# Kernel optimization log

Measured on AMD Instinct MI355X. Metric: run time of the kernel, lower is better.

## Reference

```python
import jax, jax.numpy as jnp
import numpy as np

BN_EPS = 1e-5


def _bn_relu(h, gamma, beta):
    # BatchNorm1d in training mode: normalize over (batch, length) per channel
    mean = h.mean(axis=(0, 2), keepdims=True)
    var = h.var(axis=(0, 2), keepdims=True)
    h = (h - mean) * jax.lax.rsqrt(var + BN_EPS)
    h = h * gamma[None, :, None] + beta[None, :, None]
    return jax.nn.relu(h)


def _gather(ldesc, idx):
    # ldesc: [B, D, N], idx: [B, M] -> [B, D, M]
    B, D, N = ldesc.shape
    M = idx.shape[1]
    return jnp.take_along_axis(ldesc, jnp.broadcast_to(idx[:, None, :], (B, D, M)), axis=2)


def _scatter_mean(src, idx, N):
    # per-batch scatter-mean: src [B, D, M], idx [B, M] -> [B, D, N]
    def one(s, i):
        D = s.shape[0]
        sums = jnp.zeros((D, N), s.dtype).at[:, i].add(s)
        cnts = jnp.zeros((N,), s.dtype).at[i].add(1.0)
        return sums / jnp.maximum(cnts, 1.0)[None, :]
    return jax.vmap(one)(src, idx)


def _endpoint_update(ldesc, line_enc, idx, W1, b1, g1, bt1, W2, b2):
    B, D, _ = ldesc.shape
    ld = _gather(ldesc, idx)                                   # [B, D, 2L]
    # flip endpoint pairs: neighbor endpoint of each endpoint
    neigh = ld.reshape(B, D, -1, 2)[..., ::-1].reshape(B, D, -1)
    msg = jnp.concatenate([ld, neigh, line_enc], axis=1)       # [B, 3D, 2L]
    h = jnp.einsum('oc,bcm->bom', W1, msg) + b1[None, :, None]  # Conv1d k=1
    h = _bn_relu(h, g1, bt1)
    out = jnp.einsum('oc,bcm->bom', W2, h) + b2[None, :, None]
    return out                                                  # [B, D, 2L]


def setup_inputs() -> dict:
    key = jax.random.key(0)
    ks = jax.random.split(key, 12)
    B, D, N, M = 8, 256, 8192, 8192
    inp = {
        'ldesc0': jax.random.normal(ks[0], (B, D, N), jnp.float32),
        'ldesc1': jax.random.normal(ks[1], (B, D, N), jnp.float32),
        'line_enc0': jax.random.normal(ks[2], (B, D, M), jnp.float32),
        'line_enc1': jax.random.normal(ks[3], (B, D, M), jnp.float32),
        'lines_junc_idx0': jax.random.randint(ks[4], (B, M), 0, N),
        'lines_junc_idx1': jax.random.randint(ks[5], (B, M), 0, N),
        'W1': jax.random.normal(ks[6], (2 * D, 3 * D), jnp.float32) * (1.0 / np.sqrt(3 * D)),
        'b1': jnp.zeros((2 * D,), jnp.float32),
        'g1': jnp.ones((2 * D,), jnp.float32),
        'bt1': jnp.zeros((2 * D,), jnp.float32),
        'W2': jax.random.normal(ks[7], (D, 2 * D), jnp.float32) * (1.0 / np.sqrt(2 * D)),
        'b2': jnp.zeros((D,), jnp.float32),
    }
    return inp


def reference(ldesc0, ldesc1, line_enc0, line_enc1, lines_junc_idx0, lines_junc_idx1,
              W1, b1, g1, bt1, W2, b2):
    N = ldesc0.shape[2]
    up0 = _endpoint_update(ldesc0, line_enc0, lines_junc_idx0, W1, b1, g1, bt1, W2, b2)
    up1 = _endpoint_update(ldesc1, line_enc1, lines_junc_idx1, W1, b1, g1, bt1, W2, b2)
    out0 = ldesc0 + _scatter_mean(up0, lines_junc_idx0, N)
    out1 = ldesc1 + _scatter_mean(up1, lines_junc_idx1, N)
    return (out0, out1)
```

## Files before the change

### kernel.cpp

```cpp
#include <hip/hip_runtime.h>
#include <hip/hip_bf16.h>

#define B_  8
#define D_  256
#define N_  8192
#define M_  8192
#define O1_ 512
#define K1_ 768
#define K2_ 512

typedef unsigned short u16;
typedef __attribute__((ext_vector_type(8))) short bf8;
typedef __attribute__((ext_vector_type(4))) float f4;

static __device__ __forceinline__ float bf2f(u16 u) {
    unsigned v = ((unsigned)u) << 16;
    return __uint_as_float(v);
}
static __device__ __forceinline__ u16 f2bf(float f) {
    __hip_bfloat16 h = __float2bfloat16(f);
    return *reinterpret_cast<u16*>(&h);
}
static __device__ __forceinline__ void gl_lds16(const u16* g, u16* l) {
    __builtin_amdgcn_global_load_lds((const __attribute__((address_space(1))) void*)g,
                                     (__attribute__((address_space(3))) void*)l, 16, 0, 0);
}
static __device__ __forceinline__ int swz64(int r) {
    return (((r >> 1) & 1) << 4) | (((r >> 2) & 1) << 5);
}

__global__ __launch_bounds__(256) void k_transpose_bf16(const float* __restrict__ src,
                                                        u16* __restrict__ dst, int R, int C) {
    __shared__ float t[32][33];
    const int b  = blockIdx.z;
    const int c0 = blockIdx.x * 32, r0 = blockIdx.y * 32;
    const int tx = threadIdx.x, ty = threadIdx.y;
    const float* s = src + (size_t)b * R * C;
    u16* d = dst + (size_t)b * C * R;
#pragma unroll
    for (int i = 0; i < 4; ++i) {
        int r = r0 + ty + i * 8;
        t[ty + i * 8][tx] = s[(size_t)r * C + (c0 + tx)];
    }
    __syncthreads();
#pragma unroll
    for (int i = 0; i < 4; ++i) {
        int c = c0 + ty + i * 8;
        d[(size_t)c * R + (r0 + tx)] = f2bf(t[tx][ty + i * 8]);
    }
}

__global__ __launch_bounds__(256) void k_convert_w(const float* __restrict__ W1, const float* __restrict__ W2,
                                                   u16* __restrict__ W1b, u16* __restrict__ W2b) {
    int i = blockIdx.x * 256 + threadIdx.x;
    const int n1 = O1_ * K1_;
    const int n2 = D_ * K2_;
    if (i < n1) W1b[i] = f2bf(W1[i]);
    int j = i - n1;
    if (j >= 0 && j < n2) W2b[j] = f2bf(W2[j]);
}

#define NT1 12
__global__ __launch_bounds__(512, 2) void k_gemm1(const u16* __restrict__ W1b,
                                                  const u16* __restrict__ Tld,
                                                  const u16* __restrict__ Tle,
                                                  const int* __restrict__ idx,
                                                  u16* __restrict__ hbuf) {
    __shared__ u16 LA[2][2][256][32];
    __shared__ u16 LB[2][2][256][32];
    const int b  = blockIdx.z;
    const int o0 = blockIdx.y * 256;
    const int m0 = blockIdx.x * 256;
    const int tid = threadIdx.x;
    const int w = tid >> 6, l = tid & 63;
    const int wr = w >> 2;
    const int wc = w & 3;

    const int srow   = tid >> 2;
    const int schunk = (tid & 3) * 16;

    int na[2], nb[2], mm[2];
    const u16* aS[2];
    int bcolu[2];
#pragma unroll
    for (int j = 0; j < 2; ++j) {
        int r = j * 128 + srow;
        int m = m0 + r;
        mm[j] = m;
        na[j] = idx[b * M_ + m];
        nb[j] = idx[b * M_ + (m ^ 1)];
        int swu = (schunk ^ swz64(r)) >> 1;
        aS[j]   = W1b + (size_t)(o0 + r) * K1_ + swu;
        bcolu[j] = swu;
    }

    int aOff[8], bOff[4];
#pragma unroll
    for (int i = 0; i < 8; ++i) {
        int r = wr * 128 + i * 16 + (l & 15);
        aOff[i] = r * 32 + ((((l >> 4) * 16) ^ swz64(r)) >> 1);
    }
#pragma unroll
    for (int j = 0; j < 4; ++j) {
        int r = wc * 64 + j * 16 + (l & 15);
        bOff[j] = r * 32 + ((((l >> 4) * 16) ^ swz64(r)) >> 1);
    }

#define STAGE_A1(kt, ks, buf)                                                        \
    {                                                                                \
        _Pragma("unroll")                                                            \
        for (int j = 0; j < 2; ++j)                                                  \
            gl_lds16(aS[j] + (kt) * 64 + (ks) * 32, &LA[buf][ks][j * 128][0] + tid * 8); \
    }
#define STAGE_B1(kt, ks, buf)                                                        \
    {                                                                                \
        const int seg = (kt) >> 2;                                                   \
        const int cb  = ((kt) & 3) * 64 + (ks) * 32;                                 \
        _Pragma("unroll")                                                            \
        for (int j = 0; j < 2; ++j) {                                                \
            const u16* s;                                                            \
            if (seg == 0)      s = Tld + (size_t)(b * N_ + na[j]) * D_ + cb + bcolu[j]; \
            else if (seg == 1) s = Tld + (size_t)(b * N_ + nb[j]) * D_ + cb + bcolu[j]; \
            else               s = Tle + (size_t)(b * M_ + mm[j]) * D_ + cb + bcolu[j]; \
            gl_lds16(s, &LB[buf][ks][j * 128][0] + tid * 8);                         \
        }                                                                            \
    }

    f4 acc[8][4];
#pragma unroll
    for (int i = 0; i < 8; ++i)
#pragma unroll
        for (int j = 0; j < 4; ++j) acc[i][j] = {0.f, 0.f, 0.f, 0.f};

    STAGE_A1(0, 0, 0); STAGE_B1(0, 0, 0);
    STAGE_A1(0, 1, 0); STAGE_B1(0, 1, 0);
    STAGE_A1(1, 0, 1); STAGE_B1(1, 0, 1);
    asm volatile("s_waitcnt vmcnt(8)" ::: "memory");
    __builtin_amdgcn_s_barrier();
    __builtin_amdgcn_sched_barrier(0);

    for (int t = 0; t < NT1; ++t) {
        const int bufp = t & 1, nbuf = bufp ^ 1;
        const u16* baseA0 = &LA[bufp][0][0][0];
        const u16* baseA1 = &LA[bufp][1][0][0];
        const u16* baseB0 = &LB[bufp][0][0][0];
        const u16* baseB1 = &LB[bufp][1][0][0];
        bf8 aF[4], bF[4];

#pragma unroll
        for (int j = 0; j < 4; ++j) bF[j] = *reinterpret_cast<const bf8*>(baseB0 + bOff[j]);
#pragma unroll
        for (int ii = 0; ii < 4; ++ii) aF[ii] = *reinterpret_cast<const bf8*>(baseA0 + aOff[ii]);
        if (t + 1 < NT1) STAGE_A1(t + 1, 1, nbuf);
        __builtin_amdgcn_s_barrier();
        asm volatile("s_waitcnt lgkmcnt(0)" ::: "memory");
        __builtin_amdgcn_sched_barrier(0);
        __builtin_amdgcn_s_setprio(1);
#pragma unroll
        for (int ii = 0; ii < 4; ++ii)
#pragma unroll
            for (int j = 0; j < 4; ++j)
                acc[ii][j] = __builtin_amdgcn_mfma_f32_16x16x32_bf16(aF[ii], bF[j], acc[ii][j], 0, 0, 0);
        __builtin_amdgcn_s_setprio(0);
        __builtin_amdgcn_s_barrier();
        __builtin_amdgcn_sched_barrier(0);

#pragma unroll
        for (int ii = 0; ii < 4; ++ii) aF[ii] = *reinterpret_cast<const bf8*>(baseA0 + aOff[4 + ii]);
        if (t + 1 < NT1) STAGE_B1(t + 1, 1, nbuf);
        __builtin_amdgcn_s_barrier();
        asm volatile("s_waitcnt lgkmcnt(0)" ::: "memory");
        __builtin_amdgcn_sched_barrier(0);
        __builtin_amdgcn_s_setprio(1);
#pragma unroll
        for (int ii = 0; ii < 4; ++ii)
#pragma unroll
            for (int j = 0; j < 4; ++j)
                acc[4 + ii][j] = __builtin_amdgcn_mfma_f32_16x16x32_bf16(aF[ii], bF[j], acc[4 + ii][j], 0, 0, 0);
        __builtin_amdgcn_s_setprio(0);
        if (t < NT1 - 2) asm volatile("s_waitcnt vmcnt(8)" ::: "memory");
        else             asm volatile("s_waitcnt vmcnt(0)" ::: "memory");
        __builtin_amdgcn_s_barrier();
        __builtin_amdgcn_sched_barrier(0);

#pragma unroll
        for (int j = 0; j < 4; ++j) bF[j] = *reinterpret_cast<const bf8*>(baseB1 + bOff[j]);
#pragma unroll
        for (int ii = 0; ii < 4; ++ii) aF[ii] = *reinterpret_cast<const bf8*>(baseA1 + aOff[ii]);
        if (t + 2 < NT1) STAGE_A1(t + 2, 0, bufp);
        __builtin_amdgcn_s_barrier();
        asm volatile("s_waitcnt lgkmcnt(0)" ::: "memory");
        __builtin_amdgcn_sched_barrier(0);
        __builtin_amdgcn_s_setprio(1);
#pragma unroll
        for (int ii = 0; ii < 4; ++ii)
#pragma unroll
            for (int j = 0; j < 4; ++j)
                acc[ii][j] = __builtin_amdgcn_mfma_f32_16x16x32_bf16(aF[ii], bF[j], acc[ii][j], 0, 0, 0);
        __builtin_amdgcn_s_setprio(0);
        __builtin_amdgcn_s_barrier();
        __builtin_amdgcn_sched_barrier(0);

#pragma unroll
        for (int ii = 0; ii < 4; ++ii) aF[ii] = *reinterpret_cast<const bf8*>(baseA1 + aOff[4 + ii]);
        if (t + 2 < NT1) STAGE_B1(t + 2, 0, bufp);
        __builtin_amdgcn_s_barrier();
        asm volatile("s_waitcnt lgkmcnt(0)" ::: "memory");
        __builtin_amdgcn_sched_barrier(0);
        __builtin_amdgcn_s_setprio(1);
#pragma unroll
        for (int ii = 0; ii < 4; ++ii)
#pragma unroll
            for (int j = 0; j < 4; ++j)
                acc[4 + ii][j] = __builtin_amdgcn_mfma_f32_16x16x32_bf16(aF[ii], bF[j], acc[4 + ii][j], 0, 0, 0);
        __builtin_amdgcn_s_setprio(0);
        if (t < NT1 - 2) asm volatile("s_waitcnt vmcnt(8)" ::: "memory");
        else             asm volatile("s_waitcnt vmcnt(0)" ::: "memory");
        __builtin_amdgcn_s_barrier();
        __builtin_amdgcn_sched_barrier(0);
    }
#undef STAGE_A1
#undef STAGE_B1

#pragma unroll
    for (int j = 0; j < 4; ++j) {
        int m = m0 + wc * 64 + j * 16 + (l & 15);
        size_t rowbase = (size_t)(b * M_ + m) * O1_;
#pragma unroll
        for (int i = 0; i < 8; ++i) {
            int orow = o0 + wr * 128 + i * 16 + (l >> 4) * 4;
            ushort4 pk;
            pk.x = f2bf(acc[i][j].x);
            pk.y = f2bf(acc[i][j].y);
            pk.z = f2bf(acc[i][j].z);
            pk.w = f2bf(acc[i][j].w);
            *reinterpret_cast<ushort4*>(&hbuf[rowbase + orow]) = pk;
        }
    }
}

__global__ __launch_bounds__(256) void k_stats(const u16* __restrict__ hbuf, float* __restrict__ stats) {
    const int t = threadIdx.x;
    const size_t row0 = (size_t)blockIdx.x * 256;
    float s0 = 0.f, q0 = 0.f, s1 = 0.f, q1 = 0.f;
    for (int r = 0; r < 256; ++r) {
        const u16* p = hbuf + (row0 + r) * O1_;
        float v0 = bf2f(p[t]);
        float v1 = bf2f(p[t + 256]);
        s0 += v0; q0 += v0 * v0;
        s1 += v1; q1 += v1 * v1;
    }
    atomicAdd(&stats[t], s0);
    atomicAdd(&stats[O1_ + t], q0);
    atomicAdd(&stats[t + 256], s1);
    atomicAdd(&stats[O1_ + t + 256], q1);
}

__global__ void k_finalize_ac(const float* __restrict__ stats, const float* __restrict__ g1,
                              const float* __restrict__ bt1, float* __restrict__ ac) {
    int o = blockIdx.x * 256 + threadIdx.x;
    if (o >= O1_) return;
    const float inv = 1.0f / ((float)B_ * (float)M_);
    float mean = stats[o] * inv;
    float var  = stats[O1_ + o] * inv - mean * mean;
    var = fmaxf(var, 0.0f);
    float a = g1[o] * rsqrtf(var + 1e-5f);
    ac[o] = a;
    ac[O1_ + o] = bt1[o] - mean * a;
}

__global__ void k_count_int(const int* __restrict__ idx, int* __restrict__ cnt) {
    int i = blockIdx.x * 256 + threadIdx.x;
    if (i < B_ * M_) atomicAdd(&cnt[(i >> 13) * N_ + idx[i]], 1);
}

__global__ __launch_bounds__(1024) void k_scan(const int* __restrict__ cnt, int* __restrict__ offs,
                                               int* __restrict__ fill) {
    __shared__ int wsum[1024];
    const int b = blockIdx.x;
    const int t = threadIdx.x;
    const int base = b * N_;
    int v[8]; int s = 0;
#pragma unroll
    for (int k = 0; k < 8; ++k) { v[k] = cnt[base + t * 8 + k]; s += v[k]; }
    wsum[t] = s;
    __syncthreads();
    for (int off = 1; off < 1024; off <<= 1) {
        int add = (t >= off) ? wsum[t - off] : 0;
        __syncthreads();
        wsum[t] += add;
        __syncthreads();
    }
    int run = (t > 0) ? wsum[t - 1] : 0;
#pragma unroll
    for (int k = 0; k < 8; ++k) {
        offs[base + t * 8 + k] = run;
        fill[base + t * 8 + k] = run;
        run += v[k];
    }
}

__global__ void k_fill(const int* __restrict__ idx, int* __restrict__ fill, int* __restrict__ mlist) {
    int i = blockIdx.x * 256 + threadIdx.x;
    if (i < B_ * M_) {
        int b = i >> 13, m = i & (M_ - 1);
        int pos = atomicAdd(&fill[b * N_ + idx[i]], 1);
        mlist[(size_t)b * M_ + pos] = m;
    }
}

__global__ __launch_bounds__(256) void k_gemm2(const u16* __restrict__ W2b,
                                               const u16* __restrict__ hbuf,
                                               const float* __restrict__ ac,
                                               const float* __restrict__ b2,
                                               u16* __restrict__ up) {
    __shared__ u16 At[128 * 32];
    __shared__ u16 Bt[128 * 32];
    __shared__ float acs[1024];
    const int b  = blockIdx.z;
    const int d0 = blockIdx.y * 128;
    const int m0 = blockIdx.x * 128;
    const int tid = threadIdx.x;
    const int w = tid >> 6, l = tid & 63;
    const int lr = l >> 2, lc = (l & 3) * 8;

    acs[tid]       = ac[tid];
    acs[tid + 256] = ac[tid + 256];
    acs[tid + 512] = ac[tid + 512];
    acs[tid + 768] = ac[tid + 768];

    const u16* pA[2]; const u16* pB[2];
#pragma unroll
    for (int t = 0; t < 2; ++t) {
        int row = t * 64 + w * 16 + lr;
        pA[t] = W2b + (size_t)(d0 + row) * K2_ + lc;
        int m  = m0 + row;
        pB[t] = hbuf + (size_t)(b * M_ + m) * O1_ + lc;
    }
    const int wr = w >> 1, wc = w & 1;
    f4 acc[4][4];
#pragma unroll
    for (int i = 0; i < 4; ++i)
#pragma unroll
        for (int j = 0; j < 4; ++j) acc[i][j] = {0.f, 0.f, 0.f, 0.f};

    const int aoff = (wr * 64 + (l & 15)) * 32 + (l >> 4) * 8;
    const int boff = (wc * 64 + (l & 15)) * 32 + (l >> 4) * 8;
    const int bdst = (w * 16 + lr) * 32 + lc;

    __syncthreads();

    for (int kk = 0; kk < 16; ++kk) {
        const int o = kk * 32 + lc;
        f4 A0 = *reinterpret_cast<const f4*>(&acs[o]);
        f4 A1 = *reinterpret_cast<const f4*>(&acs[o + 4]);
        f4 C0 = *reinterpret_cast<const f4*>(&acs[512 + o]);
        f4 C1 = *reinterpret_cast<const f4*>(&acs[512 + o + 4]);
#pragma unroll
        for (int t = 0; t < 2; ++t) {
            gl_lds16(pA[t] + kk * 32, At + (t * 64 + w * 16) * 32);
            const ushort4* ps = reinterpret_cast<const ushort4*>(pB[t] + kk * 32);
            ushort4 v0 = ps[0], v1 = ps[1];
            union { ushort4 u4[2]; bf8 v8; } pk;
            pk.u4[0].x = f2bf(fmaxf(bf2f(v0.x) * A0.x + C0.x, 0.0f));
            pk.u4[0].y = f2bf(fmaxf(bf2f(v0.y) * A0.y + C0.y, 0.0f));
            pk.u4[0].z = f2bf(fmaxf(bf2f(v0.z) * A0.z + C0.z, 0.0f));
            pk.u4[0].w = f2bf(fmaxf(bf2f(v0.w) * A0.w + C0.w, 0.0f));
            pk.u4[1].x = f2bf(fmaxf(bf2f(v1.x) * A1.x + C1.x, 0.0f));
            pk.u4[1].y = f2bf(fmaxf(bf2f(v1.y) * A1.y + C1.y, 0.0f));
            pk.u4[1].z = f2bf(fmaxf(bf2f(v1.z) * A1.z + C1.z, 0.0f));
            pk.u4[1].w = f2bf(fmaxf(bf2f(v1.w) * A1.w + C1.w, 0.0f));
            *reinterpret_cast<bf8*>(&Bt[t * 64 * 32 + bdst]) = pk.v8;
        }
        __syncthreads();
        bf8 aF[4], bF[4];
#pragma unroll
        for (int i = 0; i < 4; ++i) aF[i] = *reinterpret_cast<const bf8*>(&At[aoff + i * 16 * 32]);
#pragma unroll
        for (int j = 0; j < 4; ++j) bF[j] = *reinterpret_cast<const bf8*>(&Bt[boff + j * 16 * 32]);
#pragma unroll
        for (int i = 0; i < 4; ++i)
#pragma unroll
            for (int j = 0; j < 4; ++j)
                acc[i][j] = __builtin_amdgcn_mfma_f32_16x16x32_bf16(aF[i], bF[j], acc[i][j], 0, 0, 0);
        __syncthreads();
    }

#pragma unroll
    for (int j = 0; j < 4; ++j) {
        int m = m0 + wc * 64 + j * 16 + (l & 15);
        size_t rowbase = (size_t)(b * M_ + m) * D_;
#pragma unroll
        for (int i = 0; i < 4; ++i) {
            int d = d0 + wr * 64 + i * 16 + (l >> 4) * 4;
            ushort4 pk;
            pk.x = f2bf(acc[i][j].x + b2[d + 0]);
            pk.y = f2bf(acc[i][j].y + b2[d + 1]);
            pk.z = f2bf(acc[i][j].z + b2[d + 2]);
            pk.w = f2bf(acc[i][j].w + b2[d + 3]);
            *reinterpret_cast<ushort4*>(&up[rowbase + d]) = pk;
        }
    }
}

__global__ __launch_bounds__(256) void k_reduce_finalize(const float* __restrict__ ldesc,
                                                         const u16* __restrict__ up,
                                                         const int* __restrict__ cnt,
                                                         const int* __restrict__ offs,
                                                         const int* __restrict__ mlist,
                                                         float* __restrict__ out) {
    __shared__ float lds[32][257];
    const int b  = blockIdx.z;
    const int n0 = blockIdx.x * 32;
    const int tx = threadIdx.x, ty = threadIdx.y;
#pragma unroll
    for (int i = 0; i < 4; ++i) {
        int nl = ty + i * 8;
        int n  = n0 + nl;
        int c   = cnt[b * N_ + n];
        int off = offs[b * N_ + n];
        float inv = 1.0f / (float)max(c, 1);
        float acc[8] = {0.f, 0.f, 0.f, 0.f, 0.f, 0.f, 0.f, 0.f};
        for (int e = 0; e < c; ++e) {
            int m = mlist[(size_t)b * M_ + off + e];
            const ushort4* row = reinterpret_cast<const ushort4*>(up + (size_t)(b * M_ + m) * D_ + tx * 8);
            ushort4 aa = row[0], bb = row[1];
            acc[0] += bf2f(aa.x); acc[1] += bf2f(aa.y); acc[2] += bf2f(aa.z); acc[3] += bf2f(aa.w);
            acc[4] += bf2f(bb.x); acc[5] += bf2f(bb.y); acc[6] += bf2f(bb.z); acc[7] += bf2f(bb.w);
        }
#pragma unroll
        for (int k = 0; k < 8; ++k) lds[nl][tx * 8 + k] = acc[k] * inv;
    }
    __syncthreads();
#pragma unroll
    for (int i = 0; i < 32; ++i) {
        int d = ty + i * 8;
        size_t o2 = (size_t)(b * D_ + d) * N_ + n0 + tx;
        out[o2] = ldesc[o2] + lds[tx][d];
    }
}

__global__ void k_marker(float* out, float v) { out[0] = v; }

extern "C" void kernel_launch(void* const* d_in, const int* in_sizes, int n_in,
                              void* d_out, int out_size, void* d_ws, size_t ws_size,
                              hipStream_t stream) {
    const float* ldesc0 = (const float*)d_in[0];
    const float* ldesc1 = (const float*)d_in[1];
    const float* le0    = (const float*)d_in[2];
    const float* le1    = (const float*)d_in[3];
    const int*   idx0   = (const int*)d_in[4];
    const int*   idx1   = (const int*)d_in[5];
    const float* W1     = (const float*)d_in[6];
    const float* g1     = (const float*)d_in[8];
    const float* bt1    = (const float*)d_in[9];
    const float* W2     = (const float*)d_in[10];
    const float* b2     = (const float*)d_in[11];
    float* out = (float*)d_out;

    char* ws = (char*)d_ws;
    const size_t oTld   = 0;
    const size_t oTle   = 33554432;
    const size_t oH     = 67108864;
    const size_t oW1b   = 134217728;
    const size_t oW2b   = oW1b + 786432;
    const size_t oStats = oW2b + 262144;
    const size_t oAC    = oStats + 4096;
    const size_t NEED   = oAC + 4096;
    if (ws_size < NEED) {
        k_marker<<<1, 1, 0, stream>>>(out, 1000.0f + (float)(ws_size >> 20));
        return;
    }
    u16*   Tld   = (u16*)(ws + oTld);
    u16*   up    = (u16*)(ws + oTld);
    u16*   Tle   = (u16*)(ws + oTle);
    int*   cnt   = (int*)(ws + oTle);
    int*   offs  = (int*)(ws + oTle + 262144);
    int*   fill  = (int*)(ws + oTle + 524288);
    int*   mlist = (int*)(ws + oTle + 786432);
    u16*   hbuf  = (u16*)(ws + oH);
    u16*   W1b   = (u16*)(ws + oW1b);
    u16*   W2b   = (u16*)(ws + oW2b);
    float* stats = (float*)(ws + oStats);
    float* ac    = (float*)(ws + oAC);

    k_convert_w<<<2048, 256, 0, stream>>>(W1, W2, W1b, W2b);

    const dim3 tb(32, 8);
    for (int s = 0; s < 2; ++s) {
        const float* ld  = s ? ldesc1 : ldesc0;
        const float* le  = s ? le1 : le0;
        const int*   idx = s ? idx1 : idx0;
        float* outp = out + (size_t)s * B_ * D_ * N_;

        k_transpose_bf16<<<dim3(N_ / 32, D_ / 32, B_), tb, 0, stream>>>(ld, Tld, D_, N_);
        k_transpose_bf16<<<dim3(M_ / 32, D_ / 32, B_), tb, 0, stream>>>(le, Tle, D_, M_);
        k_gemm1<<<dim3(M_ / 256, O1_ / 256, B_), 512, 0, stream>>>(W1b, Tld, Tle, idx, hbuf);
        hipMemsetAsync(stats, 0, 4096, stream);
        k_stats<<<256, 256, 0, stream>>>(hbuf, stats);
        k_finalize_ac<<<2, 256, 0, stream>>>(stats, g1, bt1, ac);
        hipMemsetAsync(cnt, 0, (size_t)B_ * N_ * 4, stream);
        k_count_int<<<B_ * M_ / 256, 256, 0, stream>>>(idx, cnt);
        k_scan<<<B_, 1024, 0, stream>>>(cnt, offs, fill);
        k_fill<<<B_ * M_ / 256, 256, 0, stream>>>(idx, fill, mlist);
        k_gemm2<<<dim3(M_ / 128, D_ / 128, B_), 256, 0, stream>>>(W2b, hbuf, ac, b2, up);
        k_reduce_finalize<<<dim3(N_ / 32, 1, B_), tb, 0, stream>>>(ld, up, cnt, offs, mlist, outp);
    }
}
```

Measured before the change: 453.4 us.

## Batch both sides into single kernel launches with doubled workspace

Replaces the two-iteration per-side loop with single launches that cover both sides through an extra grid dimension. Each kernel now picks its side from blockIdx.z, and the workspace buffers are doubled to hold both sides. This cuts the launch count roughly in half and gives larger grids, so small kernels such as scan, stats and finalize fill the GPU better. The cost is twice the workspace memory and a larger working set per kernel, which can hurt cache reuse.

Result: faster. 412.9 us (-8.9%).

```diff
diff --git a/kernel.cpp b/kernel.cpp
--- a/kernel.cpp
+++ b/kernel.cpp
@@ -29,24 +29,28 @@
     return (((r >> 1) & 1) << 4) | (((r >> 2) & 1) << 5);
 }
 
-__global__ __launch_bounds__(256) void k_transpose_bf16(const float* __restrict__ src,
-                                                        u16* __restrict__ dst, int R, int C) {
+__global__ __launch_bounds__(256) void k_transpose_all(const float* __restrict__ s0, const float* __restrict__ s1,
+                                                       const float* __restrict__ s2, const float* __restrict__ s3,
+                                                       u16* __restrict__ dA, u16* __restrict__ dB) {
     __shared__ float t[32][33];
-    const int b  = blockIdx.z;
+    const int z = blockIdx.z;
+    const int sel = z >> 3, b = z & 7;
+    const float* src = (sel == 0) ? s0 : (sel == 1) ? s1 : (sel == 2) ? s2 : s3;
+    u16* dst = ((sel < 2) ? dA : dB) + (size_t)(sel & 1) * B_ * N_ * D_;
     const int c0 = blockIdx.x * 32, r0 = blockIdx.y * 32;
     const int tx = threadIdx.x, ty = threadIdx.y;
-    const float* s = src + (size_t)b * R * C;
-    u16* d = dst + (size_t)b * C * R;
+    const float* s = src + (size_t)b * D_ * N_;
+    u16* d = dst + (size_t)b * N_ * D_;
 #pragma unroll
     for (int i = 0; i < 4; ++i) {
         int r = r0 + ty + i * 8;
-        t[ty + i * 8][tx] = s[(size_t)r * C + (c0 + tx)];
+        t[ty + i * 8][tx] = s[(size_t)r * N_ + (c0 + tx)];
     }
     __syncthreads();
 #pragma unroll
     for (int i = 0; i < 4; ++i) {
         int c = c0 + ty + i * 8;
-        d[(size_t)c * R + (r0 + tx)] = f2bf(t[tx][ty + i * 8]);
+        d[(size_t)c * D_ + (r0 + tx)] = f2bf(t[tx][ty + i * 8]);
     }
 }
 
@@ -62,13 +66,19 @@
 
 #define NT1 12
 __global__ __launch_bounds__(512, 2) void k_gemm1(const u16* __restrict__ W1b,
-                                                  const u16* __restrict__ Tld,
-                                                  const u16* __restrict__ Tle,
-                                                  const int* __restrict__ idx,
-                                                  u16* __restrict__ hbuf) {
+                                                  const u16* __restrict__ Tld2,
+                                                  const u16* __restrict__ Tle2,
+                                                  const int* __restrict__ idx0,
+                                                  const int* __restrict__ idx1,
+                                                  u16* __restrict__ hbuf2) {
     __shared__ u16 LA[2][2][256][32];
     __shared__ u16 LB[2][2][256][32];
-    const int b  = blockIdx.z;
+    const int z  = blockIdx.z;
+    const int side = z >> 3, b = z & 7;
+    const u16* Tld = Tld2 + (size_t)side * B_ * N_ * D_;
+    const u16* Tle = Tle2 + (size_t)side * B_ * N_ * D_;
+    const int* idx = side ? idx1 : idx0;
+    u16* hbuf = hbuf2 + (size_t)side * B_ * M_ * O1_;
     const int o0 = blockIdx.y * 256;
     const int m0 = blockIdx.x * 256;
     const int tid = threadIdx.x;
@@ -239,50 +249,59 @@
     }
 }
 
-__global__ __launch_bounds__(256) void k_stats(const u16* __restrict__ hbuf, float* __restrict__ stats) {
+__global__ __launch_bounds__(256) void k_stats(const u16* __restrict__ hbuf2, float* __restrict__ stats) {
+    const int side = blockIdx.x >> 8;
+    const int blk  = blockIdx.x & 255;
+    const u16* hb = hbuf2 + (size_t)side * B_ * M_ * O1_;
+    float* st = stats + side * 1024;
     const int t = threadIdx.x;
-    const size_t row0 = (size_t)blockIdx.x * 256;
+    const size_t row0 = (size_t)blk * 256;
     float s0 = 0.f, q0 = 0.f, s1 = 0.f, q1 = 0.f;
     for (int r = 0; r < 256; ++r) {
-        const u16* p = hbuf + (row0 + r) * O1_;
+        const u16* p = hb + (row0 + r) * O1_;
         float v0 = bf2f(p[t]);
         float v1 = bf2f(p[t + 256]);
         s0 += v0; q0 += v0 * v0;
         s1 += v1; q1 += v1 * v1;
     }
-    atomicAdd(&stats[t], s0);
-    atomicAdd(&stats[O1_ + t], q0);
-    atomicAdd(&stats[t + 256], s1);
-    atomicAdd(&stats[O1_ + t + 256], q1);
+    atomicAdd(&st[t], s0);
+    atomicAdd(&st[O1_ + t], q0);
+    atomicAdd(&st[t + 256], s1);
+    atomicAdd(&st[O1_ + t + 256], q1);
 }
 
 __global__ void k_finalize_ac(const float* __restrict__ stats, const float* __restrict__ g1,
                               const float* __restrict__ bt1, float* __restrict__ ac) {
-    int o = blockIdx.x * 256 + threadIdx.x;
-    if (o >= O1_) return;
+    int i = blockIdx.x * 256 + threadIdx.x;
+    if (i >= 1024) return;
+    int side = i >> 9, o = i & 511;
+    const float* st = stats + side * 1024;
     const float inv = 1.0f / ((float)B_ * (float)M_);
-    float mean = stats[o] * inv;
-    float var  = stats[O1_ + o] * inv - mean * mean;
+    float mean = st[o] * inv;
+    float var  = st[O1_ + o] * inv - mean * mean;
     var = fmaxf(var, 0.0f);
     float a = g1[o] * rsqrtf(var + 1e-5f);
-    ac[o] = a;
-    ac[O1_ + o] = bt1[o] - mean * a;
-}
-
-__global__ void k_count_int(const int* __restrict__ idx, int* __restrict__ cnt) {
+    ac[side * 1024 + o] = a;
+    ac[side * 1024 + O1_ + o] = bt1[o] - mean * a;
+}
+
+__global__ void k_count_int(const int* __restrict__ idx0, const int* __restrict__ idx1, int* __restrict__ cnt2) {
     int i = blockIdx.x * 256 + threadIdx.x;
-    if (i < B_ * M_) atomicAdd(&cnt[(i >> 13) * N_ + idx[i]], 1);
-}
-
-__global__ __launch_bounds__(1024) void k_scan(const int* __restrict__ cnt, int* __restrict__ offs,
-                                               int* __restrict__ fill) {
+    if (i < 2 * B_ * M_) {
+        int side = i >> 16, j = i & 65535;
+        const int* idx = side ? idx1 : idx0;
+        atomicAdd(&cnt2[side * B_ * N_ + (j >> 13) * N_ + idx[j]], 1);
+    }
+}
+
+__global__ __launch_bounds__(1024) void k_scan(const int* __restrict__ cnt2, int* __restrict__ offs2,
+                                               int* __restrict__ fill2) {
     __shared__ int wsum[1024];
-    const int b = blockIdx.x;
+    const int base = blockIdx.x * N_;
     const int t = threadIdx.x;
-    const int base = b * N_;
     int v[8]; int s = 0;
 #pragma unroll
-    for (int k = 0; k < 8; ++k) { v[k] = cnt[base + t * 8 + k]; s += v[k]; }
+    for (int k = 0; k < 8; ++k) { v[k] = cnt2[base + t * 8 + k]; s += v[k]; }
     wsum[t] = s;
     __syncthreads();
     for (int off = 1; off < 1024; off <<= 1) {
@@ -294,40 +313,47 @@
     int run = (t > 0) ? wsum[t - 1] : 0;
 #pragma unroll
     for (int k = 0; k < 8; ++k) {
-        offs[base + t * 8 + k] = run;
-        fill[base + t * 8 + k] = run;
+        offs2[base + t * 8 + k] = run;
+        fill2[base + t * 8 + k] = run;
         run += v[k];
     }
 }
 
-__global__ void k_fill(const int* __restrict__ idx, int* __restrict__ fill, int* __restrict__ mlist) {
+__global__ void k_fill(const int* __restrict__ idx0, const int* __restrict__ idx1,
+                       int* __restrict__ fill2, int* __restrict__ mlist2) {
     int i = blockIdx.x * 256 + threadIdx.x;
-    if (i < B_ * M_) {
-        int b = i >> 13, m = i & (M_ - 1);
-        int pos = atomicAdd(&fill[b * N_ + idx[i]], 1);
-        mlist[(size_t)b * M_ + pos] = m;
+    if (i < 2 * B_ * M_) {
+        int side = i >> 16, j = i & 65535;
+        const int* idx = side ? idx1 : idx0;
+        int b = j >> 13, m = j & (M_ - 1);
+        int pos = atomicAdd(&fill2[side * B_ * N_ + b * N_ + idx[j]], 1);
+        mlist2[(size_t)side * B_ * M_ + b * M_ + pos] = m;
     }
 }
 
 __global__ __launch_bounds__(256) void k_gemm2(const u16* __restrict__ W2b,
-                                               const u16* __restrict__ hbuf,
+                                               const u16* __restrict__ hbuf2,
                                                const float* __restrict__ ac,
                                                const float* __restrict__ b2,
-                                               u16* __restrict__ up) {
+                                               u16* __restrict__ up2) {
     __shared__ u16 At[128 * 32];
     __shared__ u16 Bt[128 * 32];
     __shared__ float acs[1024];
-    const int b  = blockIdx.z;
+    const int z = blockIdx.z;
+    const int side = z >> 3, b = z & 7;
+    const u16* hbuf = hbuf2 + (size_t)side * B_ * M_ * O1_;
+    u16* up = up2 + (size_t)side * B_ * M_ * D_;
+    const float* acp = ac + side * 1024;
     const int d0 = blockIdx.y * 128;
     const int m0 = blockIdx.x * 128;
     const int tid = threadIdx.x;
     const int w = tid >> 6, l = tid & 63;
     const int lr = l >> 2, lc = (l & 3) * 8;
 
-    acs[tid]       = ac[tid];
-    acs[tid + 256] = ac[tid + 256];
-    acs[tid + 512] = ac[tid + 512];
-    acs[tid + 768] = ac[tid + 768];
+    acs[tid]       = acp[tid];
+    acs[tid + 256] = acp[tid + 256];
+    acs[tid + 512] = acp[tid + 512];
+    acs[tid + 768] = acp[tid + 768];
 
     const u16* pA[2]; const u16* pB[2];
 #pragma unroll
@@ -403,14 +429,22 @@
     }
 }
 
-__global__ __launch_bounds__(256) void k_reduce_finalize(const float* __restrict__ ldesc,
-                                                         const u16* __restrict__ up,
-                                                         const int* __restrict__ cnt,
-                                                         const int* __restrict__ offs,
-                                                         const int* __restrict__ mlist,
+__global__ __launch_bounds__(256) void k_reduce_finalize(const float* __restrict__ ldesc0,
+                                                         const float* __restrict__ ldesc1,
+                                                         const u16* __restrict__ up2,
+                                                         const int* __restrict__ cnt2,
+                                                         const int* __restrict__ offs2,
+                                                         const int* __restrict__ mlist2,
                                                          float* __restrict__ out) {
     __shared__ float lds[32][257];
-    const int b  = blockIdx.z;
+    const int z = blockIdx.z;
+    const int side = z >> 3, b = z & 7;
+    const float* ldesc = side ? ldesc1 : ldesc0;
+    const u16* up = up2 + (size_t)side * B_ * M_ * D_;
+    const int* cnt  = cnt2  + side * B_ * N_;
+    const int* offs = offs2 + side * B_ * N_;
+    const int* mlist = mlist2 + (size_t)side * B_ * M_;
+    float* outp = out + (size_t)side * B_ * D_ * N_;
     const int n0 = blockIdx.x * 32;
     const int tx = threadIdx.x, ty = threadIdx.y;
 #pragma unroll
@@ -436,7 +470,7 @@
     for (int i = 0; i < 32; ++i) {
         int d = ty + i * 8;
         size_t o2 = (size_t)(b * D_ + d) * N_ + n0 + tx;
-        out[o2] = ldesc[o2] + lds[tx][d];
+        outp[o2] = ldesc[o2] + lds[tx][d];
     }
 }
 
@@ -459,26 +493,27 @@
     float* out = (float*)d_out;
 
     char* ws = (char*)d_ws;
-    const size_t oTld   = 0;
-    const size_t oTle   = 33554432;
-    const size_t oH     = 67108864;
-    const size_t oW1b   = 134217728;
+    const size_t SIDE_BND = (size_t)B_ * N_ * D_ * 2;
+    const size_t oTld2  = 0;
+    const size_t oTle2  = 2 * SIDE_BND;
+    const size_t oH2    = 4 * SIDE_BND;
+    const size_t oW1b   = oH2 + (size_t)2 * B_ * M_ * O1_ * 2;
     const size_t oW2b   = oW1b + 786432;
     const size_t oStats = oW2b + 262144;
-    const size_t oAC    = oStats + 4096;
-    const size_t NEED   = oAC + 4096;
+    const size_t oAC    = oStats + 8192;
+    const size_t NEED   = oAC + 8192;
     if (ws_size < NEED) {
         k_marker<<<1, 1, 0, stream>>>(out, 1000.0f + (float)(ws_size >> 20));
         return;
     }
-    u16*   Tld   = (u16*)(ws + oTld);
-    u16*   up    = (u16*)(ws + oTld);
-    u16*   Tle   = (u16*)(ws + oTle);
-    int*   cnt   = (int*)(ws + oTle);
-    int*   offs  = (int*)(ws + oTle + 262144);
-    int*   fill  = (int*)(ws + oTle + 524288);
-    int*   mlist = (int*)(ws + oTle + 786432);
-    u16*   hbuf  = (u16*)(ws + oH);
+    u16*   Tld2  = (u16*)(ws + oTld2);
+    u16*   up2   = (u16*)(ws + oTld2);
+    u16*   Tle2  = (u16*)(ws + oTle2);
+    int*   cnt2  = (int*)(ws + oTle2);
+    int*   offs2 = (int*)(ws + oTle2 + 524288);
+    int*   fill2 = (int*)(ws + oTle2 + 1048576);
+    int*   mlist2= (int*)(ws + oTle2 + 1572864);
+    u16*   hbuf2 = (u16*)(ws + oH2);
     u16*   W1b   = (u16*)(ws + oW1b);
     u16*   W2b   = (u16*)(ws + oW2b);
     float* stats = (float*)(ws + oStats);
@@ -487,23 +522,15 @@
     k_convert_w<<<2048, 256, 0, stream>>>(W1, W2, W1b, W2b);
 
     const dim3 tb(32, 8);
-    for (int s = 0; s < 2; ++s) {
-        const float* ld  = s ? ldesc1 : ldesc0;
-        const float* le  = s ? le1 : le0;
-        const int*   idx = s ? idx1 : idx0;
-        float* outp = out + (size_t)s * B_ * D_ * N_;
-
-        k_transpose_bf16<<<dim3(N_ / 32, D_ / 32, B_), tb, 0, stream>>>(ld, Tld, D_, N_);
-        k_transpose_bf16<<<dim3(M_ / 32, D_ / 32, B_), tb, 0, stream>>>(le, Tle, D_, M_);
-        k_gemm1<<<dim3(M_ / 256, O1_ / 256, B_), 512, 0, stream>>>(W1b, Tld, Tle, idx, hbuf);
-        hipMemsetAsync(stats, 0, 4096, stream);
-        k_stats<<<256, 256, 0, stream>>>(hbuf, stats);
-        k_finalize_ac<<<2, 256, 0, stream>>>(stats, g1, bt1, ac);
-        hipMemsetAsync(cnt, 0, (size_t)B_ * N_ * 4, stream);
-        k_count_int<<<B_ * M_ / 256, 256, 0, stream>>>(idx, cnt);
-        k_scan<<<B_, 1024, 0, stream>>>(cnt, offs, fill);
-        k_fill<<<B_ * M_ / 256, 256, 0, stream>>>(idx, fill, mlist);
-        k_gemm2<<<dim3(M_ / 128, D_ / 128, B_), 256, 0, stream>>>(W2b, hbuf, ac, b2, up);
-        k_reduce_finalize<<<dim3(N_ / 32, 1, B_), tb, 0, stream>>>(ld, up, cnt, offs, mlist, outp);
-    }
-}
+    k_transpose_all<<<dim3(N_ / 32, D_ / 32, 32), tb, 0, stream>>>(ldesc0, ldesc1, le0, le1, Tld2, Tle2);
+    k_gemm1<<<dim3(M_ / 256, O1_ / 256, 16), 512, 0, stream>>>(W1b, Tld2, Tle2, idx0, idx1, hbuf2);
+    hipMemsetAsync(stats, 0, 8192, stream);
+    k_stats<<<512, 256, 0, stream>>>(hbuf2, stats);
+    k_finalize_ac<<<4, 256, 0, stream>>>(stats, g1, bt1, ac);
+    hipMemsetAsync(cnt2, 0, (size_t)2 * B_ * N_ * 4, stream);
+    k_count_int<<<2 * B_ * M_ / 256, 256, 0, stream>>>(idx0, idx1, cnt2);
+    k_scan<<<16, 1024, 0, stream>>>(cnt2, offs2, fill2);
+    k_fill<<<2 * B_ * M_ / 256, 256, 0, stream>>>(idx0, idx1, fill2, mlist2);
+    k_gemm2<<<dim3(M_ / 128, D_ / 128, 16), 256, 0, stream>>>(W2b, hbuf2, ac, b2, up2);
+    k_reduce_finalize<<<dim3(N_ / 32, 1, 16), tb, 0, stream>>>(ldesc0, ldesc1, up2, cnt2, offs2, mlist2, out);
+}
```
